# Optimization experiments

Hardware: AMD Instinct MI355X
Metric: run time of the kernel (lower is better)

Reference implementation:

```python
import jax, jax.numpy as jnp
import numpy as np

NNZ = 819200
NUM_SESS = 16384
ITEMS_NUM = 1000000
EMB_DIM = 64


def setup_inputs() -> dict:
    key = jax.random.key(0)
    k1, k2, k3, k4 = jax.random.split(key, 4)
    row_idx = jnp.sort(jax.random.randint(k1, (NNZ,), 0, NUM_SESS, dtype=jnp.int32))
    col_idx = jax.random.randint(k2, (NNZ,), 0, ITEMS_NUM, dtype=jnp.int32)
    data_tensor = jax.random.uniform(k3, (NNZ,), dtype=jnp.float32)
    embeddings = jax.random.normal(k4, (ITEMS_NUM, EMB_DIM), dtype=jnp.float32)
    return {
        "row_idx": row_idx,
        "col_idx": col_idx,
        "data_tensor": data_tensor,
        "num_ids": NUM_SESS,
        "embeddings": embeddings,
    }


def reference(row_idx, col_idx, data_tensor, num_ids, embeddings):
    # sparse_coo([num_ids, ITEMS_NUM]) @ embeddings
    # == per-session weighted sum of gathered item embeddings.
    gathered = embeddings[col_idx]                      # [nnz, d]
    weighted = gathered * data_tensor[:, None]          # [nnz, d]
    user_embeddings = jax.ops.segment_sum(
        weighted, row_idx, num_segments=num_ids)        # [num_ids, d]
    return user_embeddings
```

## Files before the change

kernel.cpp:

```cpp
#include <hip/hip_runtime.h>


__global__ __launch_bounds__(256) void build_rowptr_kernel(
    const int* __restrict__ row_idx,
    int*       __restrict__ row_ptr,
    int nnz, int num_sess)
{
    int j = blockIdx.x * blockDim.x + threadIdx.x;
    if (j >= nnz) return;
    int r = row_idx[j];
    if (j == 0) {
        for (int s = 0; s <= r; ++s) row_ptr[s] = 0;
    } else {
        int rp = row_idx[j - 1];
        for (int s = rp + 1; s <= r; ++s) row_ptr[s] = j;
    }
    if (j == nnz - 1) {
        for (int s = r + 1; s <= num_sess; ++s) row_ptr[s] = nnz;
    }
}

__global__ __launch_bounds__(256, 8) void wsum_sess_kernel(
    const int*    __restrict__ row_ptr,
    const int*    __restrict__ col_idx,
    const float*  __restrict__ data,
    const float4* __restrict__ emb,
    float4*       __restrict__ out,
    int num_sess)
{
    const int wave = threadIdx.x >> 6;
    const int lane = threadIdx.x & 63;
    const int sess = (blockIdx.x << 2) + wave;
    if (sess >= num_sess) return;

    const int start = row_ptr[sess];
    const int end   = row_ptr[sess + 1];

    const int r = lane >> 4;
    const int c = lane & 15;

    float4 acc = make_float4(0.f, 0.f, 0.f, 0.f);

    int j0 = start;
    for (; j0 + 16 <= end; j0 += 16) {
        int   c0 = col_idx[j0 + 0  + r];
        int   c1 = col_idx[j0 + 4  + r];
        int   c2 = col_idx[j0 + 8  + r];
        int   c3 = col_idx[j0 + 12 + r];
        float w0 = data[j0 + 0  + r];
        float w1 = data[j0 + 4  + r];
        float w2 = data[j0 + 8  + r];
        float w3 = data[j0 + 12 + r];
        float4 e0 = emb[((size_t)c0 << 4) + c];
        float4 e1 = emb[((size_t)c1 << 4) + c];
        float4 e2 = emb[((size_t)c2 << 4) + c];
        float4 e3 = emb[((size_t)c3 << 4) + c];
        acc.x += w0 * e0.x + w1 * e1.x + w2 * e2.x + w3 * e3.x;
        acc.y += w0 * e0.y + w1 * e1.y + w2 * e2.y + w3 * e3.y;
        acc.z += w0 * e0.z + w1 * e1.z + w2 * e2.z + w3 * e3.z;
        acc.w += w0 * e0.w + w1 * e1.w + w2 * e2.w + w3 * e3.w;
    }
    for (; j0 < end; j0 += 4) {
        int   j     = j0 + r;
        bool  valid = (j < end);
        int   col   = valid ? col_idx[j] : 0;
        float w     = valid ? data[j]    : 0.f;
        float4 e = emb[((size_t)col << 4) + c];
        acc.x += w * e.x;
        acc.y += w * e.y;
        acc.z += w * e.z;
        acc.w += w * e.w;
    }

    acc.x += __shfl_xor(acc.x, 16, 64);
    acc.y += __shfl_xor(acc.y, 16, 64);
    acc.z += __shfl_xor(acc.z, 16, 64);
    acc.w += __shfl_xor(acc.w, 16, 64);
    acc.x += __shfl_xor(acc.x, 32, 64);
    acc.y += __shfl_xor(acc.y, 32, 64);
    acc.z += __shfl_xor(acc.z, 32, 64);
    acc.w += __shfl_xor(acc.w, 32, 64);

    if (r == 0)
        out[((size_t)sess << 4) + c] = acc;
}

extern "C" void kernel_launch(void* const* d_in, const int* in_sizes, int n_in,
                              void* d_out, int out_size, void* d_ws, size_t ws_size,
                              hipStream_t stream) {
    const int*   row_idx = (const int*)  d_in[0];
    const int*   col_idx = (const int*)  d_in[1];
    const float* data    = (const float*)d_in[2];
    const float* emb     = (const float*)d_in[4];

    const int nnz      = in_sizes[0];
    const int num_sess = out_size / 64;

    int* row_ptr = (int*)d_ws;

    build_rowptr_kernel<<<(nnz + 255) / 256, 256, 0, stream>>>(
        row_idx, row_ptr, nnz, num_sess);

    const int blocks = (num_sess + 3) / 4;
    wsum_sess_kernel<<<blocks, 256, 0, stream>>>(
        row_ptr, col_idx, data, (const float4*)emb, (float4*)d_out,
        num_sess);
}
```

Measured before the change: 337.6 us.

## Fuse row-pointer build into gather kernel via per-wave binary search

Removes the separate row_ptr construction kernel. Each wave now binary-searches the sorted row_idx array to find its session's start and end, using two lanes for the two bounds. The tail loop becomes a single unrolled 4-step block, and the output store is nontemporal. This saves a kernel launch and a global round trip through row_ptr. In exchange, every wave does about 20 dependent global loads before it can start gathering.

Measured after the change: 346.8 us. +2.7%, slower.

```diff
diff --git a/kernel.cpp b/kernel.cpp
--- a/kernel.cpp
+++ b/kernel.cpp
@@ -1,40 +1,30 @@
 #include <hip/hip_runtime.h>
 
 
-__global__ __launch_bounds__(256) void build_rowptr_kernel(
-    const int* __restrict__ row_idx,
-    int*       __restrict__ row_ptr,
-    int nnz, int num_sess)
-{
-    int j = blockIdx.x * blockDim.x + threadIdx.x;
-    if (j >= nnz) return;
-    int r = row_idx[j];
-    if (j == 0) {
-        for (int s = 0; s <= r; ++s) row_ptr[s] = 0;
-    } else {
-        int rp = row_idx[j - 1];
-        for (int s = rp + 1; s <= r; ++s) row_ptr[s] = j;
-    }
-    if (j == nnz - 1) {
-        for (int s = r + 1; s <= num_sess; ++s) row_ptr[s] = nnz;
-    }
-}
+typedef float nfloat4 __attribute__((ext_vector_type(4)));
 
-__global__ __launch_bounds__(256, 8) void wsum_sess_kernel(
-    const int*    __restrict__ row_ptr,
+__global__ __launch_bounds__(256, 8) void wsum_fused_kernel(
+    const int*    __restrict__ row_idx,
     const int*    __restrict__ col_idx,
     const float*  __restrict__ data,
     const float4* __restrict__ emb,
     float4*       __restrict__ out,
-    int num_sess)
+    int num_sess, int nnz)
 {
     const int wave = threadIdx.x >> 6;
     const int lane = threadIdx.x & 63;
     const int sess = (blockIdx.x << 2) + wave;
     if (sess >= num_sess) return;
 
-    const int start = row_ptr[sess];
-    const int end   = row_ptr[sess + 1];
+    int target = sess + (lane & 1);
+    int lo = 0, hi = nnz;
+    while (lo < hi) {
+        int mid = (lo + hi) >> 1;
+        int v = row_idx[mid];
+        if (v < target) lo = mid + 1; else hi = mid;
+    }
+    const int start = __shfl(lo, 0, 64);
+    const int end   = __shfl(lo, 1, 64);
 
     const int r = lane >> 4;
     const int c = lane & 15;
@@ -60,16 +50,19 @@
         acc.z += w0 * e0.z + w1 * e1.z + w2 * e2.z + w3 * e3.z;
         acc.w += w0 * e0.w + w1 * e1.w + w2 * e2.w + w3 * e3.w;
     }
-    for (; j0 < end; j0 += 4) {
-        int   j     = j0 + r;
-        bool  valid = (j < end);
-        int   col   = valid ? col_idx[j] : 0;
-        float w     = valid ? data[j]    : 0.f;
-        float4 e = emb[((size_t)col << 4) + c];
-        acc.x += w * e.x;
-        acc.y += w * e.y;
-        acc.z += w * e.z;
-        acc.w += w * e.w;
+    if (j0 < end) {
+        #pragma unroll
+        for (int k = 0; k < 4; ++k) {
+            int   j     = j0 + (k << 2) + r;
+            bool  valid = (j < end);
+            int   col   = valid ? col_idx[j] : 0;
+            float w     = valid ? data[j]    : 0.f;
+            float4 e = emb[((size_t)col << 4) + c];
+            acc.x += w * e.x;
+            acc.y += w * e.y;
+            acc.z += w * e.z;
+            acc.w += w * e.w;
+        }
     }
 
     acc.x += __shfl_xor(acc.x, 16, 64);
@@ -81,8 +74,11 @@
     acc.z += __shfl_xor(acc.z, 32, 64);
     acc.w += __shfl_xor(acc.w, 32, 64);
 
-    if (r == 0)
-        out[((size_t)sess << 4) + c] = acc;
+    if (r == 0) {
+        nfloat4 v = { acc.x, acc.y, acc.z, acc.w };
+        __builtin_nontemporal_store(
+            v, (nfloat4*)&out[((size_t)sess << 4) + c]);
+    }
 }
 
 extern "C" void kernel_launch(void* const* d_in, const int* in_sizes, int n_in,
@@ -96,13 +92,10 @@
     const int nnz      = in_sizes[0];
     const int num_sess = out_size / 64;
 
-    int* row_ptr = (int*)d_ws;
-
-    build_rowptr_kernel<<<(nnz + 255) / 256, 256, 0, stream>>>(
-        row_idx, row_ptr, nnz, num_sess);
+    (void)d_ws; (void)ws_size;
 
     const int blocks = (num_sess + 3) / 4;
-    wsum_sess_kernel<<<blocks, 256, 0, stream>>>(
-        row_ptr, col_idx, data, (const float4*)emb, (float4*)d_out,
-        num_sess);
+    wsum_fused_kernel<<<blocks, 256, 0, stream>>>(
+        row_idx, col_idx, data, (const float4*)emb, (float4*)d_out,
+        num_sess, nnz);
 }
```
